# Kernel optimization log

Measured on AMD Instinct MI355X. Metric: run time of the kernel, lower is better.

The kernel has to match this reference:

```python
import jax, jax.numpy as jnp
import numpy as np

B, T, D, H = 2, 2048, 1024, 16
HD = D // H
REG = 16
WIN = 256
ROPE_BASE = 10000.0


def _rope_cos_sin(t, hd):
    theta = 1.0 / (ROPE_BASE ** (jnp.arange(0, hd, 2, dtype=jnp.float32) / hd))  # [hd/2]
    idx_theta = jnp.arange(t, dtype=jnp.float32)[:, None] * theta[None, :]       # [T, hd/2]
    return jnp.cos(idx_theta), jnp.sin(idx_theta)


def _apply_rope(x, cos, sin):
    # x: [B, T, H, HD]
    xs = x.reshape(*x.shape[:-1], HD // 2, 2)
    x0, x1 = xs[..., 0], xs[..., 1]
    c = cos[None, :, None, :]
    s = sin[None, :, None, :]
    out = jnp.stack([x0 * c - x1 * s, x1 * c + x0 * s], axis=-1)
    return out.reshape(x.shape)


def _keep_mask(t):
    # Faithful to _build_attention_register_mask: True = attend (SDPA bool semantics).
    i = jnp.arange(t)[:, None]
    j = jnp.arange(t)[None, :]
    half = WIN // 2
    window_block = (i >= REG) & (j >= jnp.maximum(REG, i - half)) & (j <= i + half)
    blocked = (j < REG) | (i < REG) | window_block
    return ~blocked  # [T, T] bool


def setup_inputs() -> dict:
    key = jax.random.key(0)
    k1, k2, k3 = jax.random.split(key, 3)
    x = jax.random.normal(k1, (B, T, D), dtype=jnp.float32)
    w_attn = jax.random.normal(k2, (3 * D, D), dtype=jnp.float32) * 0.02  # torch Linear weight [out,in]
    w_proj = jax.random.normal(k3, (D, D), dtype=jnp.float32) * 0.02
    return {"x": x, "w_attn": w_attn, "w_proj": w_proj}


def reference(x, w_attn, w_proj):
    b, t, d = x.shape
    qkv = jnp.einsum('btd,ed->bte', x, w_attn)               # [B,T,3D]
    q, k, v = jnp.split(qkv, 3, axis=-1)
    q = q.reshape(b, t, H, HD)
    k = k.reshape(b, t, H, HD)
    v = v.reshape(b, t, H, HD)
    cos, sin = _rope_cos_sin(t, HD)
    q = _apply_rope(q, cos, sin)
    k = _apply_rope(k, cos, sin)
    q = q.transpose(0, 2, 1, 3)  # [B,H,T,HD]
    k = k.transpose(0, 2, 1, 3)
    v = v.transpose(0, 2, 1, 3)
    keep = _keep_mask(t)
    scores = jnp.einsum('bhqd,bhkd->bhqk', q, k) / jnp.sqrt(jnp.float32(HD))
    scores = jnp.where(keep[None, None], scores, -jnp.inf)
    # safe softmax (fully-masked rows -> 0, matching SDPA efficient backends)
    m = jnp.max(scores, axis=-1, keepdims=True)
    m = jnp.where(jnp.isfinite(m), m, 0.0)
    e = jnp.exp(scores - m)
    s = jnp.sum(e, axis=-1, keepdims=True)
    probs = e / jnp.maximum(s, 1e-20)
    y = jnp.einsum('bhqk,bhkd->bhqd', probs, v)
    y = y.transpose(0, 2, 1, 3).reshape(b, t, d)
    return jnp.einsum('btd,ed->bte', y, w_proj)
```

## Files before the change

### kernel.cpp

```cpp
#include <hip/hip_runtime.h>
#include <hip/hip_bf16.h>

#define DEV static __device__ __forceinline__

typedef __attribute__((ext_vector_type(8))) short bf16x8;
typedef __attribute__((ext_vector_type(4))) short bf16x4;
typedef __attribute__((ext_vector_type(4))) float f32x4;

#define MFMA16(a, b, c) __builtin_amdgcn_mfma_f32_16x16x32_bf16((a), (b), (c), 0, 0, 0)

DEV f32x4 pv_mfma(bf16x4 a, bf16x4 b, f32x4 c) {
#if __has_builtin(__builtin_amdgcn_mfma_f32_16x16x16_bf16)
  return __builtin_amdgcn_mfma_f32_16x16x16_bf16(a, b, c, 0, 0, 0);
#elif __has_builtin(__builtin_amdgcn_mfma_f32_16x16x16bf16_1k)
  return __builtin_amdgcn_mfma_f32_16x16x16bf16_1k(a, b, c, 0, 0, 0);
#else
  f32x4 d;
  asm volatile("v_mfma_f32_16x16x16_bf16 %0, %1, %2, %3"
               : "=v"(d) : "v"(a), "v"(b), "v"(c));
  return d;
#endif
}

DEV bf16x4 pk4(float e0, float e1, float e2, float e3) {
  unsigned lo, hi;
  asm("v_cvt_pk_bf16_f32 %0, %1, %2" : "=v"(lo) : "v"(e0), "v"(e1));
  asm("v_cvt_pk_bf16_f32 %0, %1, %2" : "=v"(hi) : "v"(e2), "v"(e3));
  union { unsigned u[2]; bf16x4 v; } r;
  r.u[0] = lo; r.u[1] = hi;
  return r.v;
}

#define B_ 2
#define T_ 2048
#define D_ 1024
#define H_ 16
#define HD_ 64
#define LOG2E 1.4426950408889634f

DEV short f2bf(float f) {
  union { float f; unsigned u; } w; w.f = f;
  unsigned u = w.u + 0x7fffu + ((w.u >> 16) & 1u);
  return (short)(u >> 16);
}

DEV void gld16(const void* g, void* l) {
  __builtin_amdgcn_global_load_lds(
      (const __attribute__((address_space(1))) void*)g,
      (__attribute__((address_space(3))) void*)l, 16, 0, 0);
}

#define XN 4194304
#define WAN 3145728
__global__ void cvt_k(const float* __restrict__ x, const float* __restrict__ wa,
                      const float* __restrict__ wp, short* __restrict__ xb,
                      short* __restrict__ wab, short* __restrict__ wpb) {
  size_t gi = ((size_t)blockIdx.x * 256 + threadIdx.x) * 8;
  const float* src; short* dst;
  if (gi < XN) { src = x + gi; dst = xb + gi; }
  else if (gi < XN + WAN) { src = wa + (gi - XN); dst = wab + (gi - XN); }
  else { src = wp + (gi - XN - WAN); dst = wpb + (gi - XN - WAN); }
  float4 a = *(const float4*)src;
  float4 b = *(const float4*)(src + 4);
  bf16x8 o;
  o[0] = f2bf(a.x); o[1] = f2bf(a.y); o[2] = f2bf(a.z); o[3] = f2bf(a.w);
  o[4] = f2bf(b.x); o[5] = f2bf(b.y); o[6] = f2bf(b.z); o[7] = f2bf(b.w);
  *(bf16x8*)dst = o;
}

__global__ void rope_table_k(float2* __restrict__ tab) {
  int i = blockIdx.x * 256 + threadIdx.x;
  if (i >= T_ * 32) return;
  int t = i >> 5, d = i & 31;
  float theta = powf(10000.0f, -(float)(2 * d) / 64.0f);
  float a = (float)t * theta;
  tab[i] = make_float2(cosf(a), sinf(a));
}

#define GEMM_CORE(Aptr, Bptr, KDIM)                                              \
  __shared__ short aT[128 * 64];                                                 \
  __shared__ short bT[128 * 64];                                                 \
  const int tid = threadIdx.x;                                                   \
  const int lane = tid & 63, w = tid >> 6;                                       \
  const int l15 = lane & 15, lg = lane >> 4;                                     \
  const int wr = w >> 1, wc = w & 1;                                             \
  const int mBase = blockIdx.y * 128, nBase = blockIdx.x * 128;                  \
  const int lrow = lane >> 3;                                                    \
  const int gch = (lane & 7) ^ lrow;                                             \
  const short* Asrc = (Aptr) + (size_t)(mBase + w * 32 + lrow) * (KDIM) + gch * 8;\
  const short* Bsrc = (Bptr) + (size_t)(nBase + w * 32 + lrow) * (KDIM) + gch * 8;\
  short* aDst = aT + w * 2048;                                                   \
  short* bDst = bT + w * 2048;                                                   \
  f32x4 acc[4][4];                                                               \
  _Pragma("unroll") for (int i = 0; i < 4; ++i)                                  \
  _Pragma("unroll") for (int j = 0; j < 4; ++j)                                  \
      acc[i][j] = (f32x4){0.f, 0.f, 0.f, 0.f};                                   \
  const int nk = (KDIM) / 64;                                                    \
  for (int kt = 0; kt < nk; ++kt) {                                              \
    if (kt) __syncthreads();                                                     \
    _Pragma("unroll") for (int p = 0; p < 4; ++p) {                              \
      gld16(Asrc + kt * 64 + p * 8 * (KDIM), aDst + p * 512);                    \
      gld16(Bsrc + kt * 64 + p * 8 * (KDIM), bDst + p * 512);                    \
    }                                                                            \
    __syncthreads();                \
    bf16x8 af[4][2], bfv[4][2];                                                  \
    _Pragma("unroll") for (int i = 0; i < 4; ++i)                                \
    _Pragma("unroll") for (int s = 0; s < 2; ++s) {                              \
      const int ra = wr * 64 + i * 16 + l15;                                     \
      const int rb = wc * 64 + i * 16 + l15;                                     \
      af[i][s] = *(const bf16x8*)&aT[ra * 64 + (((4 * s + lg) ^ (ra & 7)) * 8)]; \
      bfv[i][s] = *(const bf16x8*)&bT[rb * 64 + (((4 * s + lg) ^ (rb & 7)) * 8)];\
    }                                                                            \
    _Pragma("unroll") for (int mi = 0; mi < 4; ++mi)                             \
    _Pragma("unroll") for (int ni = 0; ni < 4; ++ni)                             \
    _Pragma("unroll") for (int s = 0; s < 2; ++s)                                \
        acc[mi][ni] = MFMA16(af[mi][s], bfv[ni][s], acc[mi][ni]);                \
  }

__global__ void gemm_qkv_k(const short* __restrict__ Xb, const short* __restrict__ Wb,
                           short* __restrict__ Q, short* __restrict__ Ko,
                           short* __restrict__ Vt, const float2* __restrict__ tab) {
  GEMM_CORE(Xb, Wb, 1024)

  const int sec = nBase >> 10;
#pragma unroll
  for (int mi = 0; mi < 4; ++mi) {
    const int m0 = mBase + wr * 64 + mi * 16 + lg * 4;
#pragma unroll
    for (int ni = 0; ni < 4; ++ni) {
      const int n = nBase + wc * 64 + ni * 16 + l15;
      const int hd = n & 63;
      const int h = (n >> 6) & 15;
      if (sec < 2) {
        short* dst = (sec == 0) ? Q : Ko;
        const float qscale = (sec == 0) ? (0.125f * LOG2E) : 1.0f;
#pragma unroll
        for (int r = 0; r < 4; ++r) {
          int m = m0 + r; int b = m >> 11; int t = m & 2047;
          float v = acc[mi][ni][r];
          float pv = __shfl_xor(v, 1);
          float2 cs = tab[t * 32 + (hd >> 1)];
          float o = (lane & 1) ? (v * cs.x + pv * cs.y) : (v * cs.x - pv * cs.y);
          o *= qscale;
          dst[(((size_t)b * H_ + h) * T_ + t) * HD_ + hd] = f2bf(o);
        }
      } else {
        int b = m0 >> 11; int t0 = m0 & 2047;
        short4 s4;
        s4.x = f2bf(acc[mi][ni][0]); s4.y = f2bf(acc[mi][ni][1]);
        s4.z = f2bf(acc[mi][ni][2]); s4.w = f2bf(acc[mi][ni][3]);
        *(short4*)&Vt[(((size_t)b * H_ + h) * HD_ + hd) * T_ + t0] = s4;
      }
    }
  }
}

__global__ __launch_bounds__(256, 4) void attn_k(const short* __restrict__ Qg,
                                                 const short* __restrict__ Kg,
                                                 const short* __restrict__ Vg,
                                                 short* __restrict__ Y) {
  __shared__ short kLds[64 * 72];
  __shared__ short vLds[64 * 72];
  const int tid = threadIdx.x;
  const int lane = tid & 63, w = tid >> 6;
  const int l15 = lane & 15, lg = lane >> 4;
  const int bid = blockIdx.x;
  const int wg = ((bid & 7) << 7) | (bid >> 3);
  const int qt = wg & 31, bh = wg >> 5;
  const int b = bh >> 4, h = bh & 15;
  const int q0 = qt * 64;
  const short* Qh = Qg + (size_t)bh * T_ * HD_;
  const short* Kh = Kg + (size_t)bh * T_ * HD_;
  const short* Vh = Vg + (size_t)bh * HD_ * T_;

  const int qrow = q0 + w * 16 + l15;
  bf16x8 qb[2];
  qb[0] = *(const bf16x8*)&Qh[(size_t)qrow * HD_ + lg * 8];
  qb[1] = *(const bf16x8*)&Qh[(size_t)qrow * HD_ + 32 + lg * 8];

  f32x4 ot[4];
#pragma unroll
  for (int i = 0; i < 4; ++i) ot[i] = (f32x4){0.f, 0.f, 0.f, 0.f};
  float lsum = 0.f;

  const int sRow = tid >> 3, sC = (tid & 7) * 8;
  bf16x8 kreg[2], vreg[2];
  auto issueLoad = [&](int kt) {
    const int k0 = kt * 64;
#pragma unroll
    for (int p = 0; p < 2; ++p) {
      const int row = sRow + p * 32;
      kreg[p] = *(const bf16x8*)&Kh[(size_t)(k0 + row) * HD_ + sC];
      vreg[p] = *(const bf16x8*)&Vh[(size_t)row * T_ + k0 + sC];
    }
  };
  auto inBand = [&](int kt) { const int k0 = kt * 64; return k0 >= q0 - 65 && k0 <= q0 + 65; };

  const int NT = T_ / 64;
  int kt = 0;
  while (kt < NT && inBand(kt)) ++kt;
  issueLoad(kt);

  while (kt < NT) {
    int ktn = kt + 1;
    while (ktn < NT && inBand(ktn)) ++ktn;

    __syncthreads();
#pragma unroll
    for (int p = 0; p < 2; ++p) {
      *(bf16x8*)&kLds[(sRow + p * 32) * 72 + sC] = kreg[p];
      *(bf16x8*)&vLds[(sRow + p * 32) * 72 + sC] = vreg[p];
    }
    if (ktn < NT) issueLoad(ktn);
    asm volatile("s_waitcnt lgkmcnt(0)" ::: "memory");
    __builtin_amdgcn_s_barrier();

    const int k0 = kt * 64;
    const bool clean = (q0 >= 16) && (k0 >= 16) &&
                       ((k0 + 63 < q0 - 128) || (k0 > q0 + 63 + 128));

    f32x4 s[4];
#pragma unroll
    for (int i = 0; i < 4; ++i) s[i] = (f32x4){0.f, 0.f, 0.f, 0.f};
    __builtin_amdgcn_s_setprio(1);
#pragma unroll
    for (int nf = 0; nf < 4; ++nf)
#pragma unroll
      for (int ks = 0; ks < 2; ++ks) {
        bf16x8 ka = *(const bf16x8*)&kLds[(nf * 16 + l15) * 72 + ks * 32 + lg * 8];
        s[nf] = MFMA16(ka, qb[ks], s[nf]);
      }
    __builtin_amdgcn_s_setprio(0);

    bf16x4 pf[4];
#pragma unroll
    for (int nf = 0; nf < 4; ++nf) {
      float e[4];
#pragma unroll
      for (int r = 0; r < 4; ++r) {
        if (!clean) {
          const int j = k0 + nf * 16 + lg * 4 + r;
          const bool keep = (qrow >= 16) && (j >= 16) &&
                            ((j < qrow - 128) || (j > qrow + 128));
          if (!keep) s[nf][r] = -__builtin_inff();
        }
        e[r] = __builtin_amdgcn_exp2f(s[nf][r]);
        lsum += e[r];
      }
      pf[nf] = pk4(e[0], e[1], e[2], e[3]);
    }

    __builtin_amdgcn_s_setprio(1);
#pragma unroll
    for (int kk = 0; kk < 4; ++kk) {
      bf16x4 va[4];
#pragma unroll
      for (int dt = 0; dt < 4; ++dt)
        va[dt] = *(const bf16x4*)&vLds[(dt * 16 + l15) * 72 + kk * 16 + lg * 4];
#pragma unroll
      for (int dt = 0; dt < 4; ++dt)
        ot[dt] = pv_mfma(va[dt], pf[kk], ot[dt]);
    }
    __builtin_amdgcn_s_setprio(0);
    kt = ktn;
  }

  float l = lsum;
  l += __shfl_xor(l, 16);
  l += __shfl_xor(l, 32);
  const float rl = 1.0f / fmaxf(l, 1e-20f);

  __syncthreads();
  short* tl = kLds + w * (16 * 72);
#pragma unroll
  for (int dt = 0; dt < 4; ++dt) {
    short4 s4;
    s4.x = f2bf(ot[dt][0] * rl);
    s4.y = f2bf(ot[dt][1] * rl);
    s4.z = f2bf(ot[dt][2] * rl);
    s4.w = f2bf(ot[dt][3] * rl);
    *(short4*)&tl[l15 * 72 + dt * 16 + lg * 4] = s4;
  }
  const int rr = lane >> 3, cc = (lane & 7) * 8;
#pragma unroll
  for (int hf = 0; hf < 2; ++hf) {
    const int row = hf * 8 + rr;
    bf16x8 v = *(const bf16x8*)&tl[row * 72 + cc];
    const int t = q0 + w * 16 + row;
    *(bf16x8*)&Y[((size_t)(b * T_ + t)) * D_ + h * HD_ + cc] = v;
  }
}

__global__ void gemm_proj_k(const short* __restrict__ Yg, const short* __restrict__ Wb,
                            float* __restrict__ Out) {
  GEMM_CORE(Yg, Wb, 1024)

#pragma unroll
  for (int mi = 0; mi < 4; ++mi)
#pragma unroll
    for (int ni = 0; ni < 4; ++ni)
#pragma unroll
      for (int r = 0; r < 4; ++r)
        Out[(size_t)(mBase + wr * 64 + mi * 16 + lg * 4 + r) * 1024 +
            nBase + wc * 64 + ni * 16 + l15] = acc[mi][ni][r];
}

extern "C" void kernel_launch(void* const* d_in, const int* in_sizes, int n_in,
                              void* d_out, int out_size, void* d_ws, size_t ws_size,
                              hipStream_t stream) {
  const float* x = (const float*)d_in[0];
  const float* w_attn = (const float*)d_in[1];
  const float* w_proj = (const float*)d_in[2];
  float* out = (float*)d_out;
  char* ws = (char*)d_ws;
  char* outc = (char*)d_out;
  short* Q   = (short*)(ws);
  short* K   = (short*)(ws + (size_t)8388608);
  short* Vt  = (short*)(ws + (size_t)16777216);
  short* Y   = (short*)(ws + (size_t)25165824);
  short* Wpb = (short*)(ws + (size_t)33554432);
  short* Xb   = (short*)(outc);
  short* Wab  = (short*)(outc + (size_t)8388608);
  float2* tab = (float2*)(outc + (size_t)14680064);

  cvt_k<<<dim3(4096), dim3(256), 0, stream>>>(x, w_attn, w_proj, Xb, Wab, Wpb);
  rope_table_k<<<dim3(256), dim3(256), 0, stream>>>(tab);
  gemm_qkv_k<<<dim3(24, 32), dim3(256), 0, stream>>>(Xb, Wab, Q, K, Vt, tab);
  attn_k<<<dim3(B_ * H_ * (T_ / 64)), dim3(256), 0, stream>>>(Q, K, Vt, Y);
  gemm_proj_k<<<dim3(8, 32), dim3(256), 0, stream>>>(Y, Wpb, out);
}
```

Measured before the change: 145.6 us.

## Split attention key tiles across two warp groups and fuse rope table into cvt

The attention kernel now runs 512 threads per block. Two groups of four waves each process alternating 64-key tiles from a 128-key pair loaded into double LDS buffers. At the end, group 1 writes its partial output and row sums to LDS, and group 0 reduces them and writes Y. This halves the serial loop length per block and adds a cross-group reduction plus larger LDS use. The RoPE table computation is also folded into the conversion kernel to drop one launch.

```diff
diff --git a/kernel.cpp b/kernel.cpp
--- a/kernel.cpp
+++ b/kernel.cpp
@@ -54,7 +54,8 @@
 #define WAN 3145728
 __global__ void cvt_k(const float* __restrict__ x, const float* __restrict__ wa,
                       const float* __restrict__ wp, short* __restrict__ xb,
-                      short* __restrict__ wab, short* __restrict__ wpb) {
+                      short* __restrict__ wab, short* __restrict__ wpb,
+                      float2* __restrict__ tab) {
   size_t gi = ((size_t)blockIdx.x * 256 + threadIdx.x) * 8;
   const float* src; short* dst;
   if (gi < XN) { src = x + gi; dst = xb + gi; }
@@ -66,15 +67,13 @@
   o[0] = f2bf(a.x); o[1] = f2bf(a.y); o[2] = f2bf(a.z); o[3] = f2bf(a.w);
   o[4] = f2bf(b.x); o[5] = f2bf(b.y); o[6] = f2bf(b.z); o[7] = f2bf(b.w);
   *(bf16x8*)dst = o;
-}
-
-__global__ void rope_table_k(float2* __restrict__ tab) {
-  int i = blockIdx.x * 256 + threadIdx.x;
-  if (i >= T_ * 32) return;
-  int t = i >> 5, d = i & 31;
-  float theta = powf(10000.0f, -(float)(2 * d) / 64.0f);
-  float a = (float)t * theta;
-  tab[i] = make_float2(cosf(a), sinf(a));
+  if (blockIdx.x < 256) {
+    int i = blockIdx.x * 256 + threadIdx.x;
+    int t = i >> 5, d = i & 31;
+    float theta = powf(10000.0f, -(float)(2 * d) / 64.0f);
+    float ang = (float)t * theta;
+    tab[i] = make_float2(cosf(ang), sinf(ang));
+  }
 }
 
 #define GEMM_CORE(Aptr, Bptr, KDIM)                                              \
@@ -155,14 +154,16 @@
   }
 }
 
-__global__ __launch_bounds__(256, 4) void attn_k(const short* __restrict__ Qg,
+#define HB 4608
+__global__ __launch_bounds__(512, 4) void attn_k(const short* __restrict__ Qg,
                                                  const short* __restrict__ Kg,
                                                  const short* __restrict__ Vg,
                                                  short* __restrict__ Y) {
-  __shared__ short kLds[64 * 72];
-  __shared__ short vLds[64 * 72];
+  __shared__ short kB[2 * HB];
+  __shared__ short vB[2 * HB];
   const int tid = threadIdx.x;
   const int lane = tid & 63, w = tid >> 6;
+  const int g = w >> 2, wl = w & 3;
   const int l15 = lane & 15, lg = lane >> 4;
   const int bid = blockIdx.x;
   const int wg = ((bid & 7) << 7) | (bid >> 3);
@@ -173,7 +174,7 @@
   const short* Kh = Kg + (size_t)bh * T_ * HD_;
   const short* Vh = Vg + (size_t)bh * HD_ * T_;
 
-  const int qrow = q0 + w * 16 + l15;
+  const int qrow = q0 + wl * 16 + l15;
   bf16x8 qb[2];
   qb[0] = *(const bf16x8*)&Qh[(size_t)qrow * HD_ + lg * 8];
   qb[1] = *(const bf16x8*)&Qh[(size_t)qrow * HD_ + 32 + lg * 8];
@@ -185,109 +186,134 @@
 
   const int sRow = tid >> 3, sC = (tid & 7) * 8;
   bf16x8 kreg[2], vreg[2];
-  auto issueLoad = [&](int kt) {
-    const int k0 = kt * 64;
+  auto issueLoad = [&](int pi) {
+    const int k0p = pi * 128;
 #pragma unroll
     for (int p = 0; p < 2; ++p) {
-      const int row = sRow + p * 32;
-      kreg[p] = *(const bf16x8*)&Kh[(size_t)(k0 + row) * HD_ + sC];
-      vreg[p] = *(const bf16x8*)&Vh[(size_t)row * T_ + k0 + sC];
+      kreg[p] = *(const bf16x8*)&Kh[(size_t)(k0p + p * 64 + sRow) * HD_ + sC];
+      vreg[p] = *(const bf16x8*)&Vh[(size_t)sRow * T_ + k0p + p * 64 + sC];
     }
   };
-  auto inBand = [&](int kt) { const int k0 = kt * 64; return k0 >= q0 - 65 && k0 <= q0 + 65; };
-
-  const int NT = T_ / 64;
-  int kt = 0;
-  while (kt < NT && inBand(kt)) ++kt;
-  issueLoad(kt);
-
-  while (kt < NT) {
-    int ktn = kt + 1;
-    while (ktn < NT && inBand(ktn)) ++ktn;
+  auto bannedTile = [&](int kt) { const int k0 = kt * 64; return k0 >= q0 - 65 && k0 <= q0 + 65; };
+  auto pairBanned = [&](int pi) { return bannedTile(2 * pi) && bannedTile(2 * pi + 1); };
+
+  const int NP = T_ / 128;
+  int pi = 0;
+  while (pi < NP && pairBanned(pi)) ++pi;
+  issueLoad(pi);
+
+  while (pi < NP) {
+    int pn = pi + 1;
+    while (pn < NP && pairBanned(pn)) ++pn;
 
     __syncthreads();
 #pragma unroll
     for (int p = 0; p < 2; ++p) {
-      *(bf16x8*)&kLds[(sRow + p * 32) * 72 + sC] = kreg[p];
-      *(bf16x8*)&vLds[(sRow + p * 32) * 72 + sC] = vreg[p];
-    }
-    if (ktn < NT) issueLoad(ktn);
+      *(bf16x8*)&kB[p * HB + sRow * 72 + sC] = kreg[p];
+      *(bf16x8*)&vB[p * HB + sRow * 72 + sC] = vreg[p];
+    }
+    if (pn < NP) issueLoad(pn);
     asm volatile("s_waitcnt lgkmcnt(0)" ::: "memory");
     __builtin_amdgcn_s_barrier();
 
-    const int k0 = kt * 64;
-    const bool clean = (q0 >= 16) && (k0 >= 16) &&
-                       ((k0 + 63 < q0 - 128) || (k0 > q0 + 63 + 128));
-
-    f32x4 s[4];
-#pragma unroll
-    for (int i = 0; i < 4; ++i) s[i] = (f32x4){0.f, 0.f, 0.f, 0.f};
-    __builtin_amdgcn_s_setprio(1);
-#pragma unroll
-    for (int nf = 0; nf < 4; ++nf)
-#pragma unroll
-      for (int ks = 0; ks < 2; ++ks) {
-        bf16x8 ka = *(const bf16x8*)&kLds[(nf * 16 + l15) * 72 + ks * 32 + lg * 8];
-        s[nf] = MFMA16(ka, qb[ks], s[nf]);
+    const int ktg = 2 * pi + g;
+    const int k0 = ktg * 64;
+    if (!bannedTile(ktg)) {
+      const bool clean = (q0 >= 16) && (k0 >= 16) &&
+                         ((k0 + 63 < q0 - 128) || (k0 > q0 + 63 + 128));
+      const short* kb_ = kB + g * HB;
+      const short* vb_ = vB + g * HB;
+
+      f32x4 s[4];
+#pragma unroll
+      for (int i = 0; i < 4; ++i) s[i] = (f32x4){0.f, 0.f, 0.f, 0.f};
+      __builtin_amdgcn_s_setprio(1);
+#pragma unroll
+      for (int nf = 0; nf < 4; ++nf)
+#pragma unroll
+        for (int ks = 0; ks < 2; ++ks) {
+          bf16x8 ka = *(const bf16x8*)&kb_[(nf * 16 + l15) * 72 + ks * 32 + lg * 8];
+          s[nf] = MFMA16(ka, qb[ks], s[nf]);
+        }
+      __builtin_amdgcn_s_setprio(0);
+
+      bf16x4 pf[4];
+#pragma unroll
+      for (int nf = 0; nf < 4; ++nf) {
+        float e[4];
+#pragma unroll
+        for (int r = 0; r < 4; ++r) {
+          if (!clean) {
+            const int j = k0 + nf * 16 + lg * 4 + r;
+            const bool keep = (qrow >= 16) && (j >= 16) &&
+                              ((j < qrow - 128) || (j > qrow + 128));
+            if (!keep) s[nf][r] = -__builtin_inff();
+          }
+          e[r] = __builtin_amdgcn_exp2f(s[nf][r]);
+          lsum += e[r];
+        }
+        pf[nf] = pk4(e[0], e[1], e[2], e[3]);
       }
-    __builtin_amdgcn_s_setprio(0);
-
-    bf16x4 pf[4];
-#pragma unroll
-    for (int nf = 0; nf < 4; ++nf) {
-      float e[4];
-#pragma unroll
-      for (int r = 0; r < 4; ++r) {
-        if (!clean) {
-          const int j = k0 + nf * 16 + lg * 4 + r;
-          const bool keep = (qrow >= 16) && (j >= 16) &&
-                            ((j < qrow - 128) || (j > qrow + 128));
-          if (!keep) s[nf][r] = -__builtin_inff();
-        }
-        e[r] = __builtin_amdgcn_exp2f(s[nf][r]);
-        lsum += e[r];
+
+      __builtin_amdgcn_s_setprio(1);
+#pragma unroll
+      for (int kk = 0; kk < 4; ++kk) {
+        bf16x4 va[4];
+#pragma unroll
+        for (int dt = 0; dt < 4; ++dt)
+          va[dt] = *(const bf16x4*)&vb_[(dt * 16 + l15) * 72 + kk * 16 + lg * 4];
+#pragma unroll
+        for (int dt = 0; dt < 4; ++dt)
+          ot[dt] = pv_mfma(va[dt], pf[kk], ot[dt]);
       }
-      pf[nf] = pk4(e[0], e[1], e[2], e[3]);
-    }
-
-    __builtin_amdgcn_s_setprio(1);
-#pragma unroll
-    for (int kk = 0; kk < 4; ++kk) {
-      bf16x4 va[4];
-#pragma unroll
-      for (int dt = 0; dt < 4; ++dt)
-        va[dt] = *(const bf16x4*)&vLds[(dt * 16 + l15) * 72 + kk * 16 + lg * 4];
-#pragma unroll
-      for (int dt = 0; dt < 4; ++dt)
-        ot[dt] = pv_mfma(va[dt], pf[kk], ot[dt]);
-    }
-    __builtin_amdgcn_s_setprio(0);
-    kt = ktn;
+      __builtin_amdgcn_s_setprio(0);
+    }
+    pi = pn;
   }
 
   float l = lsum;
   l += __shfl_xor(l, 16);
   l += __shfl_xor(l, 32);
-  const float rl = 1.0f / fmaxf(l, 1e-20f);
 
   __syncthreads();
-  short* tl = kLds + w * (16 * 72);
-#pragma unroll
-  for (int dt = 0; dt < 4; ++dt) {
-    short4 s4;
-    s4.x = f2bf(ot[dt][0] * rl);
-    s4.y = f2bf(ot[dt][1] * rl);
-    s4.z = f2bf(ot[dt][2] * rl);
-    s4.w = f2bf(ot[dt][3] * rl);
-    *(short4*)&tl[l15 * 72 + dt * 16 + lg * 4] = s4;
-  }
-  const int rr = lane >> 3, cc = (lane & 7) * 8;
-#pragma unroll
-  for (int hf = 0; hf < 2; ++hf) {
-    const int row = hf * 8 + rr;
-    bf16x8 v = *(const bf16x8*)&tl[row * 72 + cc];
-    const int t = q0 + w * 16 + row;
-    *(bf16x8*)&Y[((size_t)(b * T_ + t)) * D_ + h * HD_ + cc] = v;
+  float* ex = (float*)kB;
+  float* exl = (float*)((char*)kB + 16384);
+  if (g == 1) {
+#pragma unroll
+    for (int dt = 0; dt < 4; ++dt)
+#pragma unroll
+      for (int j = 0; j < 4; ++j)
+        ex[wl * 1024 + (dt * 16 + lg * 4 + j) * 16 + l15] = ot[dt][j];
+    if (lane < 16) exl[wl * 16 + l15] = l;
+  }
+  __syncthreads();
+  if (g == 0) {
+#pragma unroll
+    for (int dt = 0; dt < 4; ++dt)
+#pragma unroll
+      for (int j = 0; j < 4; ++j)
+        ot[dt][j] += ex[wl * 1024 + (dt * 16 + lg * 4 + j) * 16 + l15];
+    l += exl[wl * 16 + l15];
+    const float rl = 1.0f / fmaxf(l, 1e-20f);
+
+    short* tl = (short*)vB + wl * (16 * 72);
+#pragma unroll
+    for (int dt = 0; dt < 4; ++dt) {
+      short4 s4;
+      s4.x = f2bf(ot[dt][0] * rl);
+      s4.y = f2bf(ot[dt][1] * rl);
+      s4.z = f2bf(ot[dt][2] * rl);
+      s4.w = f2bf(ot[dt][3] * rl);
+      *(short4*)&tl[l15 * 72 + dt * 16 + lg * 4] = s4;
+    }
+    const int rr = lane >> 3, cc = (lane & 7) * 8;
+#pragma unroll
+    for (int hf = 0; hf < 2; ++hf) {
+      const int row = hf * 8 + rr;
+      bf16x8 v = *(const bf16x8*)&tl[row * 72 + cc];
+      const int t = q0 + wl * 16 + row;
+      *(bf16x8*)&Y[((size_t)(b * T_ + t)) * D_ + h * HD_ + cc] = v;
+    }
   }
 }
 
@@ -323,9 +349,8 @@
   short* Wab  = (short*)(outc + (size_t)8388608);
   float2* tab = (float2*)(outc + (size_t)14680064);
 
-  cvt_k<<<dim3(4096), dim3(256), 0, stream>>>(x, w_attn, w_proj, Xb, Wab, Wpb);
-  rope_table_k<<<dim3(256), dim3(256), 0, stream>>>(tab);
+  cvt_k<<<dim3(4096), dim3(256), 0, stream>>>(x, w_attn, w_proj, Xb, Wab, Wpb, tab);
   gemm_qkv_k<<<dim3(24, 32), dim3(256), 0, stream>>>(Xb, Wab, Q, K, Vt, tab);
-  attn_k<<<dim3(B_ * H_ * (T_ / 64)), dim3(256), 0, stream>>>(Q, K, Vt, Y);
+  attn_k<<<dim3(B_ * H_ * (T_ / 64)), dim3(512), 0, stream>>>(Q, K, Vt, Y);
   gemm_proj_k<<<dim3(8, 32), dim3(256), 0, stream>>>(Y, Wpb, out);
 }
```

Result: faster. 139.7 us (-4.1%).
